# Optimization experiments

Hardware: AMD Instinct MI355X
Metric: run time of the kernel (lower is better)

## Reference

```python
import jax, jax.numpy as jnp
import numpy as np

B, W, F, H = 2048, 64, 128, 128


def setup_inputs() -> dict:
    key = jax.random.key(0)
    ks = jax.random.split(key, 23)
    n = lambda k, shape: jax.random.normal(k, shape, dtype=jnp.float32) * 0.05
    return dict(
        X=jax.random.normal(ks[0], (B, W, F), dtype=jnp.float32),
        # InputAttention: linear1 (W+2H -> W), linear2 (W -> 1)
        ia_W1=n(ks[1], (W, W + 2 * H)), ia_b1=n(ks[2], (W,)),
        ia_W2=n(ks[3], (1, W)), ia_b2=n(ks[4], (1,)),
        # encoder LSTMCell(F, H)
        enc_Wih=n(ks[5], (4 * H, F)), enc_Whh=n(ks[6], (4 * H, H)),
        enc_bih=n(ks[7], (4 * H,)), enc_bhh=n(ks[8], (4 * H,)),
        # TemporalAttention: linear1 (3H -> H), linear2 (H -> 1)
        ta_W1=n(ks[9], (H, 3 * H)), ta_b1=n(ks[10], (H,)),
        ta_W2=n(ks[11], (1, H)), ta_b2=n(ks[12], (1,)),
        # decoder LSTMCell(1, H)
        dec_Wih=n(ks[13], (4 * H, 1)), dec_Whh=n(ks[14], (4 * H, H)),
        dec_bih=n(ks[15], (4 * H,)), dec_bhh=n(ks[16], (4 * H,)),
        # output heads
        l1_W=n(ks[17], (1, 1 + H)), l1_b=n(ks[18], (1,)),
        l2_W=n(ks[19], (H, 2 * H)), l2_b=n(ks[20], (H,)),
        l3_W=n(ks[21], (1, H)), l3_b=n(ks[22], (1,)),
    )


def _lstm_cell(x, h, c, Wih, Whh, bih, bhh):
    g = x @ Wih.T + bih + h @ Whh.T + bhh
    i, f, gg, o = jnp.split(g, 4, axis=-1)
    c_new = jax.nn.sigmoid(f) * c + jax.nn.sigmoid(i) * jnp.tanh(gg)
    h_new = jax.nn.sigmoid(o) * jnp.tanh(c_new)
    return h_new, c_new


def reference(X, ia_W1, ia_b1, ia_W2, ia_b2,
              enc_Wih, enc_Whh, enc_bih, enc_bhh,
              ta_W1, ta_b1, ta_W2, ta_b2,
              dec_Wih, dec_Whh, dec_bih, dec_bhh,
              l1_W, l1_b, l2_W, l2_b, l3_W, l3_b):
    Bsz, Wlen, Fdim = X.shape
    Hdim = enc_Whh.shape[1]
    Xf = jnp.transpose(X, (2, 0, 1))  # [F, B, W] (feature-major view for input attention)

    # ---- encoder with input attention ----
    def enc_step(carry, xt):  # xt: [B, F]
        h, c = carry
        hr = jnp.broadcast_to(h[None], (Fdim, Bsz, Hdim))
        cr = jnp.broadcast_to(c[None], (Fdim, Bsz, Hdim))
        u = jnp.tanh(jnp.concatenate([Xf, hr, cr], axis=-1) @ ia_W1.T + ia_b1)  # [F,B,W]
        e = u @ ia_W2.T + ia_b2                                                  # [F,B,1]
        alpha = jax.nn.softmax(e, axis=0)[..., 0].T                              # [B,F]
        h_new, c_new = _lstm_cell(alpha * xt, h, c, enc_Wih, enc_Whh, enc_bih, enc_bhh)
        return (h_new, c_new), h_new

    z = jnp.zeros((Bsz, Hdim), dtype=X.dtype)
    (_, _), Hs = jax.lax.scan(enc_step, (z, z), jnp.transpose(X, (1, 0, 2)))  # Hs: [W,B,H]
    # dropout: eval mode (identity)

    # ---- decoder with temporal attention ----
    def dec_step(carry, _):
        d, ds, out = carry
        dr = jnp.broadcast_to(d[None], Hs.shape)
        dsr = jnp.broadcast_to(ds[None], Hs.shape)
        v = jnp.tanh(jnp.concatenate([Hs, dr, dsr], axis=-1) @ ta_W1.T + ta_b1)  # [W,B,H]
        l = v @ ta_W2.T + ta_b2                                                   # [W,B,1]
        beta = jax.nn.softmax(l, axis=0)
        ct = jnp.sum(beta * Hs, axis=0)                                           # [B,H]
        yt = jnp.concatenate([out, ct], axis=-1) @ l1_W.T + l1_b                  # [B,1]
        d_new, ds_new = _lstm_cell(yt, d, ds, dec_Wih, dec_Whh, dec_bih, dec_bhh)
        o = jnp.concatenate([ct, d_new], axis=-1) @ l2_W.T + l2_b
        out_new = jax.nn.sigmoid(o @ l3_W.T + l3_b)                               # [B,1]
        return (d_new, ds_new, out_new), None

    out0 = jnp.zeros((Bsz, 1), dtype=X.dtype)
    (_, _, output), _ = jax.lax.scan(dec_step, (z, z, out0), None, length=Wlen)
    return output
```

## Files before the change

kernel.cpp:

```cpp
#include <hip/hip_runtime.h>
#include <hip/hip_fp16.h>
#include <stdint.h>

typedef unsigned int uint;
typedef unsigned short ushort;
typedef unsigned char uchar;

#define NB 2048
#define NW 64
#define NF 128
#define NH 128

typedef __attribute__((ext_vector_type(8))) short s8v;
typedef __attribute__((ext_vector_type(8))) _Float16 h8v;
typedef __attribute__((ext_vector_type(4))) float f4v;

#define MFMA16(a, b, c) __builtin_amdgcn_mfma_f32_16x16x32_bf16((a), (b), (c), 0, 0, 0)
#define MFMAH(a, b, c)  __builtin_amdgcn_mfma_f32_16x16x32_f16((a), (b), (c), 0, 0, 0)
#define MFMA8(a, b, c)  __builtin_amdgcn_mfma_f32_16x16x32_fp8_fp8((a), (b), (c), 0, 0, 0)

union H8 { h8v v; __half2 h2[4]; uint4 u4; ushort us[8]; };
union U8 { uint2 u2; long v; };

__device__ __forceinline__ float bfl(uint u){ return __uint_as_float(u << 16); }
__device__ __forceinline__ float bfh(uint u){ return __uint_as_float(u & 0xffff0000u); }
__device__ __forceinline__ float bf2f(ushort s){ return __uint_as_float(((uint)s) << 16); }
__device__ __forceinline__ ushort f2bf(float f){
  uint u = __float_as_uint(f);
  u += 0x7fffu + ((u >> 16) & 1u);
  return (ushort)(u >> 16);
}

__device__ __forceinline__ float fast_tanh(float x){
  float e = __expf(x + x);
  return 1.f - 2.f * __builtin_amdgcn_rcpf(e + 1.f);
}
__device__ __forceinline__ float fast_sig(float x){
  return __builtin_amdgcn_rcpf(1.f + __expf(-x));
}
__device__ __forceinline__ ushort expo_h(float x){
  return __half_as_ushort(__float2half(__expf(x + x)));
}
__device__ __forceinline__ uint f2fp8x4(float a, float b, float c, float d){
  uint u = (uint)__builtin_amdgcn_cvt_pk_fp8_f32(a, b, 0, false);
  u = (uint)__builtin_amdgcn_cvt_pk_fp8_f32(c, d, (int)u, true);
  return u;
}

__device__ __forceinline__ s8v packW(const float* p){
  s8v r;
  #pragma unroll
  for (int i = 0; i < 8; ++i) r[i] = (short)f2bf(p[i]);
  return r;
}

__global__ __launch_bounds__(256) void k_upre(const float* __restrict__ X,
                                              const float* __restrict__ iaW1,
                                              ushort* __restrict__ Eenc){
  __shared__ __align__(16) float sXT[128*68];
  const int tid = threadIdx.x, lane = tid & 63, wave = tid >> 6, g = lane >> 4;
  int b = blockIdx.x;
  const float* Xb = X + (size_t)b*NW*NF;
  for (int i = tid; i < NW*NF; i += 256){
    int j = i >> 7, f = i & 127;
    sXT[f*68 + j] = Xb[i];
  }
  s8v bw[2];
  {
    int w = wave*16 + (lane & 15);
    #pragma unroll
    for (int kb = 0; kb < 2; ++kb) bw[kb] = packW(iaW1 + w*320 + kb*32 + g*8);
  }
  __syncthreads();
  ushort* outb = Eenc + (size_t)b*NF*NW;
  int w = wave*16 + (lane & 15);
  #pragma unroll
  for (int mt = 0; mt < 8; ++mt){
    int f = mt*16 + (lane & 15);
    f4v acc = {0.f,0.f,0.f,0.f};
    #pragma unroll
    for (int kb = 0; kb < 2; ++kb){
      const float* p = &sXT[f*68 + kb*32 + g*8];
      s8v a;
      #pragma unroll
      for (int i = 0; i < 8; ++i) a[i] = (short)f2bf(p[i]);
      acc = MFMA16(a, bw[kb], acc);
    }
    int fr = mt*16 + g*4;
    #pragma unroll
    for (int j = 0; j < 4; ++j) outb[(fr + j)*64 + w] = expo_h(acc[j]);
  }
}

__global__ __launch_bounds__(256) void k_vpre(const ushort* __restrict__ Hsb,
                                              const float* __restrict__ taW1,
                                              ushort* __restrict__ Edec,
                                              uchar* __restrict__ HsT8){
  __shared__ __align__(16) ushort sH[64*136];
  const int tid = threadIdx.x, lane = tid & 63, wave = tid >> 6, g = lane >> 4;
  int b = blockIdx.x;
  const ushort* Hb = Hsb + (size_t)b*NW*NH;
  for (int i = tid; i < 1024; i += 256){
    int w = i >> 4, c = i & 15;
    *(uint4*)&sH[w*136 + c*8] = *(const uint4*)(Hb + i*8);
  }
  s8v bw[2][4];
  #pragma unroll
  for (int nt = 0; nt < 2; ++nt){
    int h = wave*32 + nt*16 + (lane & 15);
    #pragma unroll
    for (int kb = 0; kb < 4; ++kb)
      bw[nt][kb] = packW(taW1 + h*384 + kb*32 + g*8);
  }
  __syncthreads();
  uchar* ho = HsT8 + (size_t)b*NH*NW;
  for (int k = 0; k < 8; ++k){
    int s = tid + 256*k;
    int h = s >> 4, w0 = (s & 15)*4;
    float f0 = bf2f(sH[(w0+0)*136 + h])*16.f;
    float f1 = bf2f(sH[(w0+1)*136 + h])*16.f;
    float f2 = bf2f(sH[(w0+2)*136 + h])*16.f;
    float f3 = bf2f(sH[(w0+3)*136 + h])*16.f;
    *(uint*)(ho + h*64 + w0) = f2fp8x4(f0, f1, f2, f3);
  }
  ushort* outb = Edec + (size_t)b*NW*NH;
  #pragma unroll
  for (int mt = 0; mt < 4; ++mt){
    s8v af[4];
    #pragma unroll
    for (int kb = 0; kb < 4; ++kb)
      af[kb] = *(const s8v*)&sH[(mt*16 + (lane&15))*136 + kb*32 + g*8];
    #pragma unroll
    for (int nt = 0; nt < 2; ++nt){
      f4v acc = {0.f,0.f,0.f,0.f};
      #pragma unroll
      for (int kb = 0; kb < 4; ++kb) acc = MFMA16(af[kb], bw[nt][kb], acc);
      int h = wave*32 + nt*16 + (lane&15);
      int wr = mt*16 + g*4;
      #pragma unroll
      for (int j = 0; j < 4; ++j) outb[(wr + j)*128 + h] = expo_h(acc[j]);
    }
  }
}

__global__ __launch_bounds__(512, 2) void k_enc(
    const float* __restrict__ X, const float* __restrict__ iaW1,
    const float* __restrict__ iab1, const float* __restrict__ iaW2,
    const float* __restrict__ encWih, const float* __restrict__ encWhh,
    const float* __restrict__ encbih, const float* __restrict__ encbhh,
    const ushort* __restrict__ Eenc, ushort* __restrict__ Hsb){
  __shared__ __align__(16) ushort sUp[65536];
  __shared__ __align__(16) ushort sAB[16*264];
  __shared__ __align__(16) ushort sXt[16*264];
  __shared__ __align__(16) ushort uhc_h[8*64];
  __shared__ __align__(16) float  xrow[8*128];

  const int tid = threadIdx.x, lane = tid & 63, wave = tid >> 6, g = lane >> 4;
  const int bbase = blockIdx.x * 8;
  const int n16 = wave*16 + (lane & 15);

  for (int i = tid; i < 16*264; i += 512){ sAB[i] = 0; sXt[i] = 0; }
  {
    const ushort* up0 = Eenc + (size_t)bbase*NF*NW;
    #pragma unroll
    for (int k = 0; k < 16; ++k){
      int c = tid + k*512;
      int f = (c >> 3) & 127, s = c & 7;
      uint4 v = *(const uint4*)(up0 + (size_t)c*8);
      *(uint4*)((char*)sUp + (c>>3)*128 + ((s ^ (f & 7)) << 4)) = v;
    }
  }
  float bias_r[4];
  #pragma unroll
  for (int gg = 0; gg < 4; ++gg)
    bias_r[gg] = encbih[gg*128 + n16] + encbhh[gg*128 + n16];
  float b1_r = iab1[n16 & 63];
  float c_r[4] = {0.f, 0.f, 0.f, 0.f};
  s8v bwC[4][8];
  #pragma unroll
  for (int gg = 0; gg < 4; ++gg){
    int j = gg*128 + n16;
    #pragma unroll
    for (int kc = 0; kc < 8; ++kc){
      const float* p = (kc < 4) ? (encWih + j*128 + kc*32) : (encWhh + j*128 + (kc-4)*32);
      bwC[gg][kc] = packW(p + g*8);
    }
  }
  s8v bwA[8];
  if (wave < 4){
    #pragma unroll
    for (int kc = 0; kc < 8; ++kc){
      int col = (kc < 4) ? (192 + kc*32) : (64 + (kc-4)*32);
      bwA[kc] = packW(iaW1 + n16*320 + col + g*8);
    }
  }
  H8 w2f[2];
  #pragma unroll
  for (int kb = 0; kb < 2; ++kb)
    #pragma unroll
    for (int i = 0; i < 8; ++i)
      w2f[kb].v[i] = (_Float16)iaW2[kb*32 + g*8 + i];
  {
    const float* Xr = X + ((size_t)(bbase + wave)*NW + 0)*NF;
    xrow[wave*128 + lane] = Xr[lane];
    xrow[wave*128 + 64 + lane] = Xr[64 + lane];
  }
  __syncthreads();

  for (int t = 0; t < NW; ++t){
    float xn0, xn1;
    {
      int tn = (t + 1) & 63;
      const float* Xr = X + ((size_t)(bbase + wave)*NW + tn)*NF;
      xn0 = Xr[lane];
      xn1 = Xr[64 + lane];
    }
    s8v aT[8];
    #pragma unroll
    for (int kc = 0; kc < 8; ++kc)
      aT[kc] = *(const s8v*)((const char*)sAB + (lane&15)*528 + kc*64 + g*16);
    if (wave < 4){
      f4v acc = {0.f,0.f,0.f,0.f};
      #pragma unroll
      for (int kc = 0; kc < 8; ++kc) acc = MFMA16(aT[kc], bwA[kc], acc);
      if (lane < 32){
        int mb = g*4;
        #pragma unroll
        for (int j = 0; j < 4; ++j) uhc_h[(mb+j)*64 + n16] = expo_h(acc[j] + b1_r);
      }
    }
    __syncthreads();

    {
      int bb = wave;
      const char* Eb = (const char*)sUp + bb*16384;
      H8 sv[2];
      #pragma unroll
      for (int kb = 0; kb < 2; ++kb)
        sv[kb].u4 = *(const uint4*)((const char*)uhc_h + bb*128 + kb*64 + g*16);
      __half2 one2 = __float2half2_rn(1.f);
      f4v Mc[8];
      #pragma unroll
      for (int ft = 0; ft < 8; ++ft){
        int f = ft*16 + (lane & 15);
        const char* rowp = Eb + f*128;
        f4v acc = {0.f,0.f,0.f,0.f};
        #pragma unroll
        for (int kb = 0; kb < 2; ++kb){
          H8 e, a;
          e.v = *(const h8v*)(rowp + (((kb*4 + g) ^ (f & 7)) << 4));
          #pragma unroll
          for (int q = 0; q < 4; ++q) a.h2[q] = h2rcp(__hfma2(e.h2[q], sv[kb].h2[q], one2));
          acc = MFMAH(a.v, w2f[kb].v, acc);
        }
        Mc[ft] = acc;
      }
      float xs[8][4]; float ssum = 0.f;
      #pragma unroll
      for (int ft = 0; ft < 8; ++ft)
        #pragma unroll
        for (int r = 0; r < 4; ++r){ float x = __expf(-2.f*Mc[ft][r]); xs[ft][r] = x; ssum += x; }
      ssum += __shfl_xor(ssum, 16, 64);
      ssum += __shfl_xor(ssum, 32, 64);
      float inv = __builtin_amdgcn_rcpf(ssum);
      if ((lane & 15) == 0){
        #pragma unroll
        for (int ft = 0; ft < 8; ++ft){
          int f0 = ft*16 + g*4;
          float4 Xv = *(const float4*)&xrow[bb*128 + f0];
          uint lo = (uint)f2bf(xs[ft][0]*inv*Xv.x) | ((uint)f2bf(xs[ft][1]*inv*Xv.y) << 16);
          uint hi = (uint)f2bf(xs[ft][2]*inv*Xv.z) | ((uint)f2bf(xs[ft][3]*inv*Xv.w) << 16);
          *(uint2*)((char*)sXt + bb*528 + f0*2) = make_uint2(lo, hi);
        }
      }
    }
    __syncthreads();

    {
      s8v aX[4];
      #pragma unroll
      for (int kc = 0; kc < 4; ++kc)
        aX[kc] = *(const s8v*)((const char*)sXt + (lane&15)*528 + kc*64 + g*16);
      f4v acc[4];
      #pragma unroll
      for (int gg = 0; gg < 4; ++gg) acc[gg] = (f4v){0.f,0.f,0.f,0.f};
      #pragma unroll
      for (int kc = 0; kc < 8; ++kc){
        s8v af = (kc < 4) ? aX[kc] : aT[kc];
        #pragma unroll
        for (int gg = 0; gg < 4; ++gg) acc[gg] = MFMA16(af, bwC[gg][kc], acc[gg]);
      }
      if (lane < 32){
        int mb = g*4;
        #pragma unroll
        for (int j = 0; j < 4; ++j){
          int m = mb + j;
          float gi = acc[0][j] + bias_r[0];
          float gf = acc[1][j] + bias_r[1];
          float gg2 = acc[2][j] + bias_r[2];
          float go = acc[3][j] + bias_r[3];
          float cold = c_r[j];
          float cn = fast_sig(gf)*cold + fast_sig(gi)*fast_tanh(gg2);
          float hn = fast_sig(go)*fast_tanh(cn);
          c_r[j] = cn;
          sAB[m*264 + n16] = f2bf(cn);
          sAB[m*264 + 128 + n16] = f2bf(hn);
          Hsb[((size_t)(bbase + m)*NW + t)*NH + n16] = f2bf(hn);
        }
      }
      xrow[wave*128 + lane] = xn0;
      xrow[wave*128 + 64 + lane] = xn1;
    }
    __syncthreads();
  }
}

__global__ __launch_bounds__(512, 2) void k_dec(
    const float* __restrict__ taW1, const float* __restrict__ tab1,
    const float* __restrict__ taW2,
    const float* __restrict__ decWih, const float* __restrict__ decWhh,
    const float* __restrict__ decbih, const float* __restrict__ decbhh,
    const float* __restrict__ l1W, const float* __restrict__ l1b,
    const float* __restrict__ l2W, const float* __restrict__ l2b,
    const float* __restrict__ l3W, const float* __restrict__ l3b,
    const ushort* __restrict__ Edec, const uchar* __restrict__ HsT8,
    float* __restrict__ out){
  __shared__ __align__(16) ushort sVp[65536];
  __shared__ __align__(16) ushort sAB[16*264];
  __shared__ __align__(16) ushort sCT[16*136];
  __shared__ __align__(16) ushort vd_h[8*128];
  __shared__ __align__(16) uchar  lb8[8*64];
  __shared__ __align__(16) float  op_s[8][8];
  __shared__ __align__(16) float  yt_s[8];

  const int tid = threadIdx.x, lane = tid & 63, wave = tid >> 6, g = lane >> 4;
  const int bbase = blockIdx.x * 8;
  const int n16 = wave*16 + (lane & 15);

  for (int i = tid; i < 16*264; i += 512) sAB[i] = 0;
  for (int i = tid; i < 16*136; i += 512) sCT[i] = 0;
  {
    const ushort* vp0 = Edec + (size_t)bbase*NW*NH;
    #pragma unroll
    for (int k = 0; k < 16; ++k){
      int c = tid + k*512;
      int w = (c >> 4) & 63, s = c & 15;
      uint4 v = *(const uint4*)(vp0 + (size_t)c*8);
      *(uint4*)((char*)sVp + (c >> 4)*256 + ((s ^ (w & 15)) << 4)) = v;
    }
  }
  float bias_r[4], wih_r[4];
  #pragma unroll
  for (int gg = 0; gg < 4; ++gg){
    bias_r[gg] = decbih[gg*128 + n16] + decbhh[gg*128 + n16];
    wih_r[gg]  = decWih[gg*128 + n16];
  }
  float tab1_r = tab1[n16];
  float l2b_r  = l2b[n16];
  float l3w_r  = l3W[n16];
  float l1w0 = l1W[0], l1b0 = l1b[0], l3b0 = l3b[0];
  float cds_r[4] = {0.f, 0.f, 0.f, 0.f};
  s8v bwA[8];
  #pragma unroll
  for (int kc = 0; kc < 8; ++kc)
    bwA[kc] = packW(taW1 + n16*384 + 128 + kc*32 + g*8);
  s8v bwD[4][4];
  #pragma unroll
  for (int gg = 0; gg < 4; ++gg){
    int j = gg*128 + n16;
    #pragma unroll
    for (int kc = 0; kc < 4; ++kc)
      bwD[gg][kc] = packW(decWhh + j*128 + kc*32 + g*8);
  }
  s8v bwF[8];
  #pragma unroll
  for (int kc = 0; kc < 8; ++kc)
    bwF[kc] = packW(l2W + n16*256 + kc*32 + g*8);
  H8 w2df[4];
  #pragma unroll
  for (int kb = 0; kb < 4; ++kb)
    #pragma unroll
    for (int i = 0; i < 8; ++i)
      w2df[kb].v[i] = (_Float16)taW2[kb*32 + g*8 + i];
  float l1w[8];
  #pragma unroll
  for (int ht = 0; ht < 8; ++ht) l1w[ht] = l1W[1 + ht*16 + (lane & 15)];
  __syncthreads();

  for (int t = 0; t < NW; ++t){
    s8v aT[8];
    #pragma unroll
    for (int kc = 0; kc < 8; ++kc)
      aT[kc] = *(const s8v*)((const char*)sAB + (lane&15)*528 + kc*64 + g*16);
    {
      f4v acc = {0.f,0.f,0.f,0.f};
      #pragma unroll
      for (int kc = 0; kc < 8; ++kc) acc = MFMA16(aT[kc], bwA[kc], acc);
      if (lane < 32){
        int mb = g*4;
        #pragma unroll
        for (int j = 0; j < 4; ++j) vd_h[(mb+j)*128 + n16] = expo_h(acc[j] + tab1_r);
      }
    }
    __syncthreads();

    {
      int bb = wave;
      const uchar* hb8 = HsT8 + (size_t)(bbase + bb)*NH*NW;
      U8 hbf[8][2];
      #pragma unroll
      for (int ht = 0; ht < 8; ++ht){
        int h = ht*16 + (lane & 15);
        hbf[ht][0].u2 = *(const uint2*)(hb8 + h*64 + g*8);
        hbf[ht][1].u2 = *(const uint2*)(hb8 + h*64 + 32 + g*8);
      }
      const char* Eb = (const char*)sVp + bb*16384;
      H8 sv[4];
      #pragma unroll
      for (int kb = 0; kb < 4; ++kb)
        sv[kb].u4 = *(const uint4*)((const char*)vd_h + bb*256 + kb*64 + g*16);
      __half2 one2 = __float2half2_rn(1.f);
      f4v Mc[4];
      #pragma unroll
      for (int wt = 0; wt < 4; ++wt){
        int w = wt*16 + (lane & 15);
        const char* rowp = Eb + w*256;
        f4v acc = {0.f,0.f,0.f,0.f};
        #pragma unroll
        for (int kb = 0; kb < 4; ++kb){
          H8 e, a;
          e.v = *(const h8v*)(rowp + (((kb*4 + g) ^ (w & 15)) << 4));
          #pragma unroll
          for (int q = 0; q < 4; ++q) a.h2[q] = h2rcp(__hfma2(e.h2[q], sv[kb].h2[q], one2));
          acc = MFMAH(a.v, w2df[kb].v, acc);
        }
        Mc[wt] = acc;
      }
      float xs[4][4]; float ssum = 0.f;
      #pragma unroll
      for (int wt = 0; wt < 4; ++wt)
        #pragma unroll
        for (int r = 0; r < 4; ++r){ float x = __expf(-2.f*Mc[wt][r]); xs[wt][r] = x; ssum += x; }
      ssum += __shfl_xor(ssum, 16, 64);
      ssum += __shfl_xor(ssum, 32, 64);
      float inv16 = 16.f * __builtin_amdgcn_rcpf(ssum);
      if ((lane & 15) == 0){
        #pragma unroll
        for (int wt = 0; wt < 4; ++wt){
          int w0 = wt*16 + g*4;
          *(uint*)(lb8 + bb*64 + w0) =
            f2fp8x4(xs[wt][0]*inv16, xs[wt][1]*inv16, xs[wt][2]*inv16, xs[wt][3]*inv16);
        }
      }
      U8 ba0, ba1;
      ba0.u2 = *(const uint2*)(lb8 + bb*64 + g*8);
      ba1.u2 = *(const uint2*)(lb8 + bb*64 + 32 + g*8);
      float p = 0.f;
      #pragma unroll
      for (int ht = 0; ht < 8; ++ht){
        f4v acc = {0.f,0.f,0.f,0.f};
        acc = MFMA8(ba0.v, hbf[ht][0].v, acc);
        acc = MFMA8(ba1.v, hbf[ht][1].v, acc);
        float ctv = acc[0] * (1.f/256.f);
        if (lane < 16) sCT[bb*136 + ht*16 + (lane&15)] = f2bf(ctv);
        p += l1w[ht] * ctv;
      }
      p += __shfl_xor(p, 1, 64);
      p += __shfl_xor(p, 2, 64);
      p += __shfl_xor(p, 4, 64);
      p += __shfl_xor(p, 8, 64);
      if (lane == 0) yt_s[bb] = p + l1b0;
    }
    __syncthreads();

    {
      f4v g4[4];
      #pragma unroll
      for (int gg = 0; gg < 4; ++gg) g4[gg] = (f4v){0.f,0.f,0.f,0.f};
      #pragma unroll
      for (int kc = 0; kc < 4; ++kc){
        #pragma unroll
        for (int gg = 0; gg < 4; ++gg) g4[gg] = MFMA16(aT[kc], bwD[gg][kc], g4[gg]);
      }
      if (lane < 32){
        int mb = g*4;
        float4 so = make_float4(0.f, 0.f, 0.f, 0.f);
        #pragma unroll
        for (int w = 0; w < 8; ++w){
          float4 v = *(const float4*)((const char*)op_s + w*32 + g*16);
          so.x += v.x; so.y += v.y; so.z += v.z; so.w += v.w;
        }
        float soa[4] = {so.x, so.y, so.z, so.w};
        #pragma unroll
        for (int j = 0; j < 4; ++j){
          int m = mb + j;
          float outp = (t == 0) ? 0.f : fast_sig(soa[j] + l3b0);
          float yt = yt_s[m] + l1w0*outp;
          float gi = g4[0][j] + bias_r[0] + wih_r[0]*yt;
          float gf = g4[1][j] + bias_r[1] + wih_r[1]*yt;
          float gg2 = g4[2][j] + bias_r[2] + wih_r[2]*yt;
          float go = g4[3][j] + bias_r[3] + wih_r[3]*yt;
          float cold = cds_r[j];
          float cn = fast_sig(gf)*cold + fast_sig(gi)*fast_tanh(gg2);
          float hn = fast_sig(go)*fast_tanh(cn);
          cds_r[j] = cn;
          sAB[m*264 + n16] = f2bf(hn);
          sAB[m*264 + 128 + n16] = f2bf(cn);
        }
      }
    }
    __syncthreads();

    {
      f4v of = {0.f,0.f,0.f,0.f};
      #pragma unroll
      for (int kc = 0; kc < 4; ++kc){
        s8v af = *(const s8v*)((const char*)sCT + (lane&15)*272 + kc*64 + g*16);
        of = MFMA16(af, bwF[kc], of);
      }
      #pragma unroll
      for (int kc = 4; kc < 8; ++kc){
        s8v af = *(const s8v*)((const char*)sAB + (lane&15)*528 + (kc-4)*64 + g*16);
        of = MFMA16(af, bwF[kc], of);
      }
      float p0 = l3w_r*(of[0] + l2b_r);
      float p1 = l3w_r*(of[1] + l2b_r);
      float p2 = l3w_r*(of[2] + l2b_r);
      float p3 = l3w_r*(of[3] + l2b_r);
      #pragma unroll
      for (int off = 1; off <= 8; off <<= 1){
        p0 += __shfl_xor(p0, off, 64);
        p1 += __shfl_xor(p1, off, 64);
        p2 += __shfl_xor(p2, off, 64);
        p3 += __shfl_xor(p3, off, 64);
      }
      if ((lane & 15) == 0 && lane < 32){
        *(float4*)((char*)op_s + wave*32 + g*16) = make_float4(p0, p1, p2, p3);
      }
    }
  }
  __syncthreads();
  if (tid < 8){
    float s = 0.f;
    #pragma unroll
    for (int w = 0; w < 8; ++w) s += op_s[w][tid];
    out[bbase + tid] = fast_sig(s + l3b0);
  }
}

extern "C" void kernel_launch(void* const* d_in, const int* in_sizes, int n_in,
                              void* d_out, int out_size, void* d_ws, size_t ws_size,
                              hipStream_t stream){
  const float* X      = (const float*)d_in[0];
  const float* iaW1   = (const float*)d_in[1];
  const float* iab1   = (const float*)d_in[2];
  const float* iaW2   = (const float*)d_in[3];
  const float* encWih = (const float*)d_in[5];
  const float* encWhh = (const float*)d_in[6];
  const float* encbih = (const float*)d_in[7];
  const float* encbhh = (const float*)d_in[8];
  const float* taW1   = (const float*)d_in[9];
  const float* tab1   = (const float*)d_in[10];
  const float* taW2   = (const float*)d_in[11];
  const float* decWih = (const float*)d_in[13];
  const float* decWhh = (const float*)d_in[14];
  const float* decbih = (const float*)d_in[15];
  const float* decbhh = (const float*)d_in[16];
  const float* l1W    = (const float*)d_in[17];
  const float* l1b    = (const float*)d_in[18];
  const float* l2W    = (const float*)d_in[19];
  const float* l2b    = (const float*)d_in[20];
  const float* l3W    = (const float*)d_in[21];
  const float* l3b    = (const float*)d_in[22];

  char* ws = (char*)d_ws;
  ushort* Eenc = (ushort*)(ws);
  ushort* Hsb  = (ushort*)(ws + 33554432);
  uchar*  HsT8 = (uchar*)(ws + 2*33554432);
  ushort* Edec = Eenc;

  k_upre<<<dim3(2048), dim3(256), 0, stream>>>(X, iaW1, Eenc);
  k_enc<<<dim3(256), dim3(512), 0, stream>>>(X, iaW1, iab1, iaW2,
                                             encWih, encWhh, encbih, encbhh,
                                             Eenc, Hsb);
  k_vpre<<<dim3(2048), dim3(256), 0, stream>>>(Hsb, taW1, Edec, HsT8);
  k_dec<<<dim3(256), dim3(512), 0, stream>>>(taW1, tab1, taW2,
                                             decWih, decWhh, decbih, decbhh,
                                             l1W, l1b, l2W, l2b, l3W, l3b,
                                             Edec, HsT8, (float*)d_out);
}
```

Baseline: 957.9 us.

## Store precomputed attention exponentials as fp8 in MFMA fragment order, read from global

```diff
diff --git a/kernel.cpp b/kernel.cpp
--- a/kernel.cpp
+++ b/kernel.cpp
@@ -14,12 +14,15 @@
 typedef __attribute__((ext_vector_type(8))) short s8v;
 typedef __attribute__((ext_vector_type(8))) _Float16 h8v;
 typedef __attribute__((ext_vector_type(4))) float f4v;
+typedef __attribute__((ext_vector_type(2))) float f2v;
+typedef __attribute__((ext_vector_type(2))) _Float16 h2v;
+typedef __attribute__((ext_vector_type(2))) __fp16 p2v;
 
 #define MFMA16(a, b, c) __builtin_amdgcn_mfma_f32_16x16x32_bf16((a), (b), (c), 0, 0, 0)
 #define MFMAH(a, b, c)  __builtin_amdgcn_mfma_f32_16x16x32_f16((a), (b), (c), 0, 0, 0)
 #define MFMA8(a, b, c)  __builtin_amdgcn_mfma_f32_16x16x32_fp8_fp8((a), (b), (c), 0, 0, 0)
 
-union H8 { h8v v; __half2 h2[4]; uint4 u4; ushort us[8]; };
+union H8 { h8v v; __half2 h2[4]; h2v hx[4]; p2v px[4]; uint4 u4; uint2 u2[2]; ushort us[8]; };
 union U8 { uint2 u2; long v; };
 
 __device__ __forceinline__ float bfl(uint u){ return __uint_as_float(u << 16); }
@@ -38,14 +41,30 @@
 __device__ __forceinline__ float fast_sig(float x){
   return __builtin_amdgcn_rcpf(1.f + __expf(-x));
 }
-__device__ __forceinline__ ushort expo_h(float x){
-  return __half_as_ushort(__float2half(__expf(x + x)));
+__device__ __forceinline__ ushort expo_hm(float x){
+  return __half_as_ushort(__float2half(__expf(x + x - 1.f)));
+}
+__device__ __forceinline__ uchar expo_fp8(float x){
+  float e = __expf(x + x + 1.f);
+  return (uchar)(__builtin_amdgcn_cvt_pk_fp8_f32(e, e, 0, false) & 0xff);
 }
 __device__ __forceinline__ uint f2fp8x4(float a, float b, float c, float d){
   uint u = (uint)__builtin_amdgcn_cvt_pk_fp8_f32(a, b, 0, false);
   u = (uint)__builtin_amdgcn_cvt_pk_fp8_f32(c, d, (int)u, true);
   return u;
 }
+__device__ __forceinline__ H8 fp8x8_to_h8(uint2 ev){
+  H8 r;
+  f2v a = __builtin_amdgcn_cvt_pk_f32_fp8((int)ev.x, false);
+  f2v b = __builtin_amdgcn_cvt_pk_f32_fp8((int)ev.x, true);
+  f2v c = __builtin_amdgcn_cvt_pk_f32_fp8((int)ev.y, false);
+  f2v d = __builtin_amdgcn_cvt_pk_f32_fp8((int)ev.y, true);
+  r.px[0] = __builtin_amdgcn_cvt_pkrtz(a.x, a.y);
+  r.px[1] = __builtin_amdgcn_cvt_pkrtz(b.x, b.y);
+  r.px[2] = __builtin_amdgcn_cvt_pkrtz(c.x, c.y);
+  r.px[3] = __builtin_amdgcn_cvt_pkrtz(d.x, d.y);
+  return r;
+}
 
 __device__ __forceinline__ s8v packW(const float* p){
   s8v r;
@@ -56,8 +75,9 @@
 
 __global__ __launch_bounds__(256) void k_upre(const float* __restrict__ X,
                                               const float* __restrict__ iaW1,
-                                              ushort* __restrict__ Eenc){
+                                              uchar* __restrict__ E8){
   __shared__ __align__(16) float sXT[128*68];
+  __shared__ __align__(16) uchar sOut[8192];
   const int tid = threadIdx.x, lane = tid & 63, wave = tid >> 6, g = lane >> 4;
   int b = blockIdx.x;
   const float* Xb = X + (size_t)b*NW*NF;
@@ -72,15 +92,14 @@
     for (int kb = 0; kb < 2; ++kb) bw[kb] = packW(iaW1 + w*320 + kb*32 + g*8);
   }
   __syncthreads();
-  ushort* outb = Eenc + (size_t)b*NF*NW;
   int w = wave*16 + (lane & 15);
   #pragma unroll
   for (int mt = 0; mt < 8; ++mt){
-    int f = mt*16 + (lane & 15);
+    int f0 = mt*16 + (lane & 15);
     f4v acc = {0.f,0.f,0.f,0.f};
     #pragma unroll
     for (int kb = 0; kb < 2; ++kb){
-      const float* p = &sXT[f*68 + kb*32 + g*8];
+      const float* p = &sXT[f0*68 + kb*32 + g*8];
       s8v a;
       #pragma unroll
       for (int i = 0; i < 8; ++i) a[i] = (short)f2bf(p[i]);
@@ -88,15 +107,23 @@
     }
     int fr = mt*16 + g*4;
     #pragma unroll
-    for (int j = 0; j < 4; ++j) outb[(fr + j)*64 + w] = expo_h(acc[j]);
-  }
+    for (int j = 0; j < 4; ++j){
+      int f = fr + j;
+      sOut[mt*1024 + (w>>5)*512 + (((w>>3)&3)*16 + (f&15))*8 + (w&7)] = expo_fp8(acc[j]);
+    }
+  }
+  __syncthreads();
+  uchar* outb = E8 + (size_t)b*8192;
+  *(uint4*)(outb + tid*32)      = *(const uint4*)(sOut + tid*32);
+  *(uint4*)(outb + tid*32 + 16) = *(const uint4*)(sOut + tid*32 + 16);
 }
 
 __global__ __launch_bounds__(256) void k_vpre(const ushort* __restrict__ Hsb,
                                               const float* __restrict__ taW1,
-                                              ushort* __restrict__ Edec,
+                                              uchar* __restrict__ E8,
                                               uchar* __restrict__ HsT8){
   __shared__ __align__(16) ushort sH[64*136];
+  __shared__ __align__(16) uchar sOut[8192];
   const int tid = threadIdx.x, lane = tid & 63, wave = tid >> 6, g = lane >> 4;
   int b = blockIdx.x;
   const ushort* Hb = Hsb + (size_t)b*NW*NH;
@@ -123,7 +150,6 @@
     float f3 = bf2f(sH[(w0+3)*136 + h])*16.f;
     *(uint*)(ho + h*64 + w0) = f2fp8x4(f0, f1, f2, f3);
   }
-  ushort* outb = Edec + (size_t)b*NW*NH;
   #pragma unroll
   for (int mt = 0; mt < 4; ++mt){
     s8v af[4];
@@ -138,9 +164,16 @@
       int h = wave*32 + nt*16 + (lane&15);
       int wr = mt*16 + g*4;
       #pragma unroll
-      for (int j = 0; j < 4; ++j) outb[(wr + j)*128 + h] = expo_h(acc[j]);
-    }
-  }
+      for (int j = 0; j < 4; ++j){
+        int w2_ = wr + j;
+        sOut[(w2_>>4)*2048 + (h>>5)*512 + (((h>>3)&3)*16 + (w2_&15))*8 + (h&7)] = expo_fp8(acc[j]);
+      }
+    }
+  }
+  __syncthreads();
+  uchar* outb = E8 + (size_t)b*8192;
+  *(uint4*)(outb + tid*32)      = *(const uint4*)(sOut + tid*32);
+  *(uint4*)(outb + tid*32 + 16) = *(const uint4*)(sOut + tid*32 + 16);
 }
 
 __global__ __launch_bounds__(512, 2) void k_enc(
@@ -148,8 +181,7 @@
     const float* __restrict__ iab1, const float* __restrict__ iaW2,
     const float* __restrict__ encWih, const float* __restrict__ encWhh,
     const float* __restrict__ encbih, const float* __restrict__ encbhh,
-    const ushort* __restrict__ Eenc, ushort* __restrict__ Hsb){
-  __shared__ __align__(16) ushort sUp[65536];
+    const uchar* __restrict__ Eenc8, ushort* __restrict__ Hsb){
   __shared__ __align__(16) ushort sAB[16*264];
   __shared__ __align__(16) ushort sXt[16*264];
   __shared__ __align__(16) ushort uhc_h[8*64];
@@ -160,16 +192,6 @@
   const int n16 = wave*16 + (lane & 15);
 
   for (int i = tid; i < 16*264; i += 512){ sAB[i] = 0; sXt[i] = 0; }
-  {
-    const ushort* up0 = Eenc + (size_t)bbase*NF*NW;
-    #pragma unroll
-    for (int k = 0; k < 16; ++k){
-      int c = tid + k*512;
-      int f = (c >> 3) & 127, s = c & 7;
-      uint4 v = *(const uint4*)(up0 + (size_t)c*8);
-      *(uint4*)((char*)sUp + (c>>3)*128 + ((s ^ (f & 7)) << 4)) = v;
-    }
-  }
   float bias_r[4];
   #pragma unroll
   for (int gg = 0; gg < 4; ++gg)
@@ -206,6 +228,8 @@
     xrow[wave*128 + 64 + lane] = Xr[64 + lane];
   }
   __syncthreads();
+
+  const uchar* Eb = Eenc8 + (size_t)(bbase + wave)*8192;
 
   for (int t = 0; t < NW; ++t){
     float xn0, xn1;
@@ -226,14 +250,13 @@
       if (lane < 32){
         int mb = g*4;
         #pragma unroll
-        for (int j = 0; j < 4; ++j) uhc_h[(mb+j)*64 + n16] = expo_h(acc[j] + b1_r);
+        for (int j = 0; j < 4; ++j) uhc_h[(mb+j)*64 + n16] = expo_hm(acc[j] + b1_r);
       }
     }
     __syncthreads();
 
     {
       int bb = wave;
-      const char* Eb = (const char*)sUp + bb*16384;
       H8 sv[2];
       #pragma unroll
       for (int kb = 0; kb < 2; ++kb)
@@ -242,13 +265,12 @@
       f4v Mc[8];
       #pragma unroll
       for (int ft = 0; ft < 8; ++ft){
-        int f = ft*16 + (lane & 15);
-        const char* rowp = Eb + f*128;
         f4v acc = {0.f,0.f,0.f,0.f};
         #pragma unroll
         for (int kb = 0; kb < 2; ++kb){
-          H8 e, a;
-          e.v = *(const h8v*)(rowp + (((kb*4 + g) ^ (f & 7)) << 4));
+          uint2 ev = *(const uint2*)(Eb + ft*1024 + kb*512 + lane*8);
+          H8 e = fp8x8_to_h8(ev);
+          H8 a;
           #pragma unroll
           for (int q = 0; q < 4; ++q) a.h2[q] = h2rcp(__hfma2(e.h2[q], sv[kb].h2[q], one2));
           acc = MFMAH(a.v, w2f[kb].v, acc);
@@ -323,9 +345,8 @@
     const float* __restrict__ l1W, const float* __restrict__ l1b,
     const float* __restrict__ l2W, const float* __restrict__ l2b,
     const float* __restrict__ l3W, const float* __restrict__ l3b,
-    const ushort* __restrict__ Edec, const uchar* __restrict__ HsT8,
+    const uchar* __restrict__ Edec8, const uchar* __restrict__ HsT8,
     float* __restrict__ out){
-  __shared__ __align__(16) ushort sVp[65536];
   __shared__ __align__(16) ushort sAB[16*264];
   __shared__ __align__(16) ushort sCT[16*136];
   __shared__ __align__(16) ushort vd_h[8*128];
@@ -339,16 +360,6 @@
 
   for (int i = tid; i < 16*264; i += 512) sAB[i] = 0;
   for (int i = tid; i < 16*136; i += 512) sCT[i] = 0;
-  {
-    const ushort* vp0 = Edec + (size_t)bbase*NW*NH;
-    #pragma unroll
-    for (int k = 0; k < 16; ++k){
-      int c = tid + k*512;
-      int w = (c >> 4) & 63, s = c & 15;
-      uint4 v = *(const uint4*)(vp0 + (size_t)c*8);
-      *(uint4*)((char*)sVp + (c >> 4)*256 + ((s ^ (w & 15)) << 4)) = v;
-    }
-  }
   float bias_r[4], wih_r[4];
   #pragma unroll
   for (int gg = 0; gg < 4; ++gg){
@@ -387,6 +398,9 @@
   for (int ht = 0; ht < 8; ++ht) l1w[ht] = l1W[1 + ht*16 + (lane & 15)];
   __syncthreads();
 
+  const uchar* Eb  = Edec8 + (size_t)(bbase + wave)*8192;
+  const uchar* hb8 = HsT8 + (size_t)(bbase + wave)*NH*NW;
+
   for (int t = 0; t < NW; ++t){
     s8v aT[8];
     #pragma unroll
@@ -399,14 +413,13 @@
       if (lane < 32){
         int mb = g*4;
         #pragma unroll
-        for (int j = 0; j < 4; ++j) vd_h[(mb+j)*128 + n16] = expo_h(acc[j] + tab1_r);
+        for (int j = 0; j < 4; ++j) vd_h[(mb+j)*128 + n16] = expo_hm(acc[j] + tab1_r);
       }
     }
     __syncthreads();
 
     {
       int bb = wave;
-      const uchar* hb8 = HsT8 + (size_t)(bbase + bb)*NH*NW;
       U8 hbf[8][2];
       #pragma unroll
       for (int ht = 0; ht < 8; ++ht){
@@ -414,7 +427,6 @@
         hbf[ht][0].u2 = *(const uint2*)(hb8 + h*64 + g*8);
         hbf[ht][1].u2 = *(const uint2*)(hb8 + h*64 + 32 + g*8);
       }
-      const char* Eb = (const char*)sVp + bb*16384;
       H8 sv[4];
       #pragma unroll
       for (int kb = 0; kb < 4; ++kb)
@@ -423,13 +435,12 @@
       f4v Mc[4];
       #pragma unroll
       for (int wt = 0; wt < 4; ++wt){
-        int w = wt*16 + (lane & 15);
-        const char* rowp = Eb + w*256;
         f4v acc = {0.f,0.f,0.f,0.f};
         #pragma unroll
         for (int kb = 0; kb < 4; ++kb){
-          H8 e, a;
-          e.v = *(const h8v*)(rowp + (((kb*4 + g) ^ (w & 15)) << 4));
+          uint2 ev = *(const uint2*)(Eb + wt*2048 + kb*512 + lane*8);
+          H8 e = fp8x8_to_h8(ev);
+          H8 a;
           #pragma unroll
           for (int q = 0; q < 4; ++q) a.h2[q] = h2rcp(__hfma2(e.h2[q], sv[kb].h2[q], one2));
           acc = MFMAH(a.v, w2df[kb].v, acc);
@@ -574,18 +585,18 @@
   const float* l3b    = (const float*)d_in[22];
 
   char* ws = (char*)d_ws;
-  ushort* Eenc = (ushort*)(ws);
-  ushort* Hsb  = (ushort*)(ws + 33554432);
-  uchar*  HsT8 = (uchar*)(ws + 2*33554432);
-  ushort* Edec = Eenc;
-
-  k_upre<<<dim3(2048), dim3(256), 0, stream>>>(X, iaW1, Eenc);
+  uchar*  Eenc8 = (uchar*)(ws);
+  ushort* Hsb   = (ushort*)(ws + 33554432);
+  uchar*  HsT8  = (uchar*)(ws + 2*33554432);
+  uchar*  Edec8 = Eenc8;
+
+  k_upre<<<dim3(2048), dim3(256), 0, stream>>>(X, iaW1, Eenc8);
   k_enc<<<dim3(256), dim3(512), 0, stream>>>(X, iaW1, iab1, iaW2,
                                              encWih, encWhh, encbih, encbhh,
-                                             Eenc, Hsb);
-  k_vpre<<<dim3(2048), dim3(256), 0, stream>>>(Hsb, taW1, Edec, HsT8);
+                                             Eenc8, Hsb);
+  k_vpre<<<dim3(2048), dim3(256), 0, stream>>>(Hsb, taW1, Edec8, HsT8);
   k_dec<<<dim3(256), dim3(512), 0, stream>>>(taW1, tab1, taW2,
                                              decWih, decWhh, decbih, decbhh,
                                              l1W, l1b, l2W, l2b, l3W, l3b,
-                                             Edec, HsT8, (float*)d_out);
-}
+                                             Edec8, HsT8, (float*)d_out);
+}
```

Result: slower. 1.570 ms (+63.9%).
